# Performance work log

Hardware: AMD Instinct MI355X
Metric: run time of the kernel (lower is better)

## Reference

```python
import jax, jax.numpy as jnp
import numpy as np

TEMPERATURE = 8.0  # sqrt(d_head=64)


def setup_inputs() -> dict:
    key = jax.random.key(0)
    ks = jax.random.split(key, 6)
    shape = (4, 16, 2048, 64)  # [B, H, L, d_head]
    names = ["q_real", "q_imag", "k_real", "k_imag", "v_real", "v_imag"]
    return {n: jax.random.normal(k, shape, dtype=jnp.float32) for n, k in zip(names, ks)}


def reference(q_real, q_imag, k_real, k_imag, v_real, v_imag):
    # attn = | (q / T) @ conj(k)^H |
    # complex matmul with b = conj(k)^T: br = k_r^T, bi = -k_i^T
    qr = q_real / TEMPERATURE
    qi = q_imag / TEMPERATURE
    # [B,H,Lq,Lk]
    s_real = jnp.einsum("bhqd,bhkd->bhqk", qr, k_real) + jnp.einsum("bhqd,bhkd->bhqk", qi, k_imag)
    s_imag = jnp.einsum("bhqd,bhkd->bhqk", qi, k_real) - jnp.einsum("bhqd,bhkd->bhqk", qr, k_imag)
    attn = jax.nn.softmax(jnp.sqrt(s_real * s_real + s_imag * s_imag), axis=-1)
    # dropout p=0.0 (eval) -> identity
    out_real = jnp.einsum("bhqk,bhkd->bhqd", attn, v_real)
    out_imag = jnp.einsum("bhqk,bhkd->bhqd", attn, v_imag)
    # torch.view_as_complex(stack([real, imag], -1)) -> represent as stacked last dim
    output = jnp.stack([out_real, out_imag], axis=-1)  # [B,H,L,d,2]
    return output, attn
```

## Files before the change

### kernel.cpp

```cpp
#include <hip/hip_runtime.h>
#include <hip/hip_bf16.h>

constexpr int kL  = 2048;
constexpr int kD  = 64;
constexpr int kBH = 64;
constexpr size_t kAttnOff = (size_t)kBH * kL * kD * 2;

typedef __bf16 bf16x8 __attribute__((ext_vector_type(8)));
typedef __bf16 bf16x4 __attribute__((ext_vector_type(4)));
typedef float  f32x4  __attribute__((ext_vector_type(4)));
typedef unsigned int u32x4 __attribute__((ext_vector_type(4)));

static __device__ inline bf16x8 neg8(bf16x8 v) {
  u32x4 t = __builtin_bit_cast(u32x4, v);
  t ^= 0x80008000u;
  return __builtin_bit_cast(bf16x8, t);
}

static __device__ inline bf16x8 pack8(const float4& a, const float4& b) {
  bf16x8 p;
  p[0]=(__bf16)a.x; p[1]=(__bf16)a.y; p[2]=(__bf16)a.z; p[3]=(__bf16)a.w;
  p[4]=(__bf16)b.x; p[5]=(__bf16)b.y; p[6]=(__bf16)b.z; p[7]=(__bf16)b.w;
  return p;
}

__global__ __launch_bounds__(256) void transpose_v_kernel(
    const float* __restrict__ vr_g, const float* __restrict__ vi_g,
    __hip_bfloat16* __restrict__ vt_r, __hip_bfloat16* __restrict__ vt_i)
{
  __shared__ __align__(16) char lds_raw[2 * 8192];
  char* tr = lds_raw;
  char* ti = lds_raw + 8192;

  const int tid = threadIdx.x;
  const int bh  = blockIdx.x >> 5;
  const int kb  = blockIdx.x & 31;
  const int k0  = kb * 64;

  {
    const int krow = tid >> 2;
    const int d0   = (tid & 3) << 4;
    const size_t gb = ((size_t)bh * kL + k0 + krow) * kD + d0;
    const int base = krow * 128;
    const int swz  = (krow & 7) << 4;
    {
      float4 x0 = *(const float4*)(vr_g + gb);
      float4 x1 = *(const float4*)(vr_g + gb + 4);
      float4 x2 = *(const float4*)(vr_g + gb + 8);
      float4 x3 = *(const float4*)(vr_g + gb + 12);
      *(bf16x8*)(tr + base + ((d0 * 2) ^ swz))      = pack8(x0, x1);
      *(bf16x8*)(tr + base + ((d0 * 2 + 16) ^ swz)) = pack8(x2, x3);
    }
    {
      float4 y0 = *(const float4*)(vi_g + gb);
      float4 y1 = *(const float4*)(vi_g + gb + 4);
      float4 y2 = *(const float4*)(vi_g + gb + 8);
      float4 y3 = *(const float4*)(vi_g + gb + 12);
      *(bf16x8*)(ti + base + ((d0 * 2) ^ swz))      = pack8(y0, y1);
      *(bf16x8*)(ti + base + ((d0 * 2 + 16) ^ swz)) = pack8(y2, y3);
    }
  }
  __syncthreads();

  {
    const int d  = tid >> 2;
    const int kc = (tid & 3) << 4;
    const size_t tb = ((size_t)bh * 32 + kb) * 8192;
    char* outr = (char*)vt_r + tb + d * 128;
    char* outi = (char*)vt_i + tb + d * 128;
    const int oswz = (d & 7) << 4;
    bf16x8 pr0, pr1, pi0, pi1;
#pragma unroll
    for (int j = 0; j < 8; ++j) {
      const int k1 = kc + j;
      const int k2 = kc + 8 + j;
      const int b1 = k1 * 128 + ((d * 2) ^ ((k1 & 7) << 4));
      const int b2 = k2 * 128 + ((d * 2) ^ ((k2 & 7) << 4));
      pr0[j] = *(const __bf16*)(tr + b1);
      pr1[j] = *(const __bf16*)(tr + b2);
      pi0[j] = *(const __bf16*)(ti + b1);
      pi1[j] = *(const __bf16*)(ti + b2);
    }
    *(bf16x8*)(outr + ((kc * 2) ^ oswz))      = pr0;
    *(bf16x8*)(outr + ((kc * 2 + 16) ^ oswz)) = pr1;
    *(bf16x8*)(outi + ((kc * 2) ^ oswz))      = pi0;
    *(bf16x8*)(outi + ((kc * 2 + 16) ^ oswz)) = pi1;
  }
}

__global__ __launch_bounds__(256, 2) void fused_all(
    const float* __restrict__ qr_g, const float* __restrict__ qi_g,
    const float* __restrict__ kr_g, const float* __restrict__ ki_g,
    const __hip_bfloat16* __restrict__ vt_r, const __hip_bfloat16* __restrict__ vt_i,
    float* __restrict__ attn, float* __restrict__ out)
{
  __shared__ __align__(16) char lds_raw[49664];
  char*  e_l   = lds_raw + 32768 + (threadIdx.x >> 6) * 4096;
  float* inv_l = (float*)(lds_raw + 49152);

  const int tid  = threadIdx.x;
  const int wave = tid >> 6;
  const int lane = tid & 63;
  const int g    = lane >> 4;
  const int r    = lane & 15;

  const int bid = blockIdx.x;
  const int nid = (bid & 7) * 128 + (bid >> 3);
  const int bh  = nid >> 4;
  const int q0w = (nid & 15) * 128 + wave * 32;

  bf16x8 aqr[2][2], aqi[2][2];
#pragma unroll
  for (int qt = 0; qt < 2; ++qt) {
    const size_t qbase = ((size_t)bh * kL + q0w + qt * 16 + r) * kD + g * 8;
#pragma unroll
    for (int f = 0; f < 2; ++f) {
      float4 x0 = *(const float4*)(qr_g + qbase + f * 32);
      float4 x1 = *(const float4*)(qr_g + qbase + f * 32 + 4);
      float4 y0 = *(const float4*)(qi_g + qbase + f * 32);
      float4 y1 = *(const float4*)(qi_g + qbase + f * 32 + 4);
      float xr[8] = {x0.x, x0.y, x0.z, x0.w, x1.x, x1.y, x1.z, x1.w};
      float xi[8] = {y0.x, y0.y, y0.z, y0.w, y1.x, y1.y, y1.z, y1.w};
#pragma unroll
      for (int i = 0; i < 8; ++i) {
        aqr[qt][f][i] = (__bf16)(xr[i] * 0.125f);
        aqi[qt][f][i] = (__bf16)(xi[i] * 0.125f);
      }
    }
  }

  const int srow = tid >> 2;
  const int sd0  = (tid & 3) << 4;

  auto STAGE_K = [&](char* buf, int krow0) {
    const size_t gb = ((size_t)bh * kL + krow0 + srow) * kD + sd0;
    const int base = srow * 128;
    const int swz  = (srow & 7) << 4;
    float4 x0 = *(const float4*)(kr_g + gb);
    float4 x1 = *(const float4*)(kr_g + gb + 4);
    float4 x2 = *(const float4*)(kr_g + gb + 8);
    float4 x3 = *(const float4*)(kr_g + gb + 12);
    float4 y0 = *(const float4*)(ki_g + gb);
    float4 y1 = *(const float4*)(ki_g + gb + 4);
    float4 y2 = *(const float4*)(ki_g + gb + 8);
    float4 y3 = *(const float4*)(ki_g + gb + 12);
    *(bf16x8*)(buf + base + ((sd0 * 2) ^ swz))             = pack8(x0, x1);
    *(bf16x8*)(buf + base + ((sd0 * 2 + 16) ^ swz))        = pack8(x2, x3);
    *(bf16x8*)(buf + 8192 + base + ((sd0 * 2) ^ swz))      = pack8(y0, y1);
    *(bf16x8*)(buf + 8192 + base + ((sd0 * 2 + 16) ^ swz)) = pack8(y2, y3);
  };

  auto QK_E = [&](const char* kr_l, const char* ki_l, int s, int qt, float e[4]) {
    const int krow = s * 16 + r;
    const int swz  = (krow & 7) << 4;
    bf16x8 bkr[2], bki[2], bkin[2];
#pragma unroll
    for (int f = 0; f < 2; ++f) {
      const int byte = krow * 128 + (((f * 32 + g * 8) * 2) ^ swz);
      bkr[f]  = *(const bf16x8*)(kr_l + byte);
      bki[f]  = *(const bf16x8*)(ki_l + byte);
      bkin[f] = neg8(bki[f]);
    }
    f32x4 accr = {0.f, 0.f, 0.f, 0.f};
    f32x4 acci = {0.f, 0.f, 0.f, 0.f};
#pragma unroll
    for (int f = 0; f < 2; ++f) {
      accr = __builtin_amdgcn_mfma_f32_16x16x32_bf16(bkr[f],  aqr[qt][f], accr, 0, 0, 0);
      accr = __builtin_amdgcn_mfma_f32_16x16x32_bf16(bki[f],  aqi[qt][f], accr, 0, 0, 0);
      acci = __builtin_amdgcn_mfma_f32_16x16x32_bf16(bkr[f],  aqi[qt][f], acci, 0, 0, 0);
      acci = __builtin_amdgcn_mfma_f32_16x16x32_bf16(bkin[f], aqr[qt][f], acci, 0, 0, 0);
    }
#pragma unroll
    for (int i = 0; i < 4; ++i)
      e[i] = __expf(sqrtf(accr[i] * accr[i] + acci[i] * acci[i]));
  };

  float rs[2] = {0.f, 0.f};

#pragma unroll 1
  for (int t = 0; t < 16; ++t) {
    __syncthreads();
#pragma unroll
    for (int c = 0; c < 2; ++c) STAGE_K(lds_raw + c * 16384, t * 128 + c * 64);
    __syncthreads();
#pragma unroll
    for (int c = 0; c < 2; ++c) {
      const char* kr_l = lds_raw + c * 16384;
      const char* ki_l = kr_l + 8192;
#pragma unroll
      for (int s = 0; s < 4; ++s) {
#pragma unroll
        for (int qt = 0; qt < 2; ++qt) {
          float e[4];
          QK_E(kr_l, ki_l, s, qt, e);
          rs[qt] += (e[0] + e[1]) + (e[2] + e[3]);
        }
      }
    }
  }

#pragma unroll
  for (int qt = 0; qt < 2; ++qt) {
    rs[qt] += __shfl_xor(rs[qt], 16, 64);
    rs[qt] += __shfl_xor(rs[qt], 32, 64);
  }
  if (lane < 16) {
    inv_l[wave * 32 + lane]      = 1.0f / rs[0];
    inv_l[wave * 32 + 16 + lane] = 1.0f / rs[1];
  }

  f32x4 o_r[2][4], o_i[2][4];
#pragma unroll
  for (int qt = 0; qt < 2; ++qt)
#pragma unroll
    for (int dt = 0; dt < 4; ++dt) {
      o_r[qt][dt] = (f32x4){0.f, 0.f, 0.f, 0.f};
      o_i[qt][dt] = (f32x4){0.f, 0.f, 0.f, 0.f};
    }

#pragma unroll 1
  for (int t = 0; t < 32; ++t) {
    const int k0 = t * 64;
    __syncthreads();
    STAGE_K(lds_raw, k0);
    {
      const size_t tb = ((size_t)bh * 32 + t) * 8192;
      const int o1 = tid * 16;
      const int o2 = o1 + 4096;
      *(u32x4*)(lds_raw + 16384 + o1) = *(const u32x4*)((const char*)vt_r + tb + o1);
      *(u32x4*)(lds_raw + 16384 + o2) = *(const u32x4*)((const char*)vt_r + tb + o2);
      *(u32x4*)(lds_raw + 24576 + o1) = *(const u32x4*)((const char*)vt_i + tb + o1);
      *(u32x4*)(lds_raw + 24576 + o2) = *(const u32x4*)((const char*)vt_i + tb + o2);
    }
    __syncthreads();

#pragma unroll
    for (int s = 0; s < 4; ++s) {
#pragma unroll
      for (int qt = 0; qt < 2; ++qt) {
        float e[4];
        QK_E(lds_raw, lds_raw + 8192, s, qt, e);
        bf16x4 pe;
#pragma unroll
        for (int i = 0; i < 4; ++i) pe[i] = (__bf16)e[i];
        const int row = qt * 16 + r;
        *(bf16x4*)(e_l + row * 128 + (((s * 16 + g * 4) * 2) ^ ((row & 7) << 4))) = pe;
      }
    }

#pragma unroll
    for (int m = 0; m < 4; ++m) {
      const int row  = m * 8 + (lane >> 3);
      const int byte = row * 128 + (((lane & 7) * 16) ^ ((row & 7) << 4));
      bf16x8 v = *(const bf16x8*)(e_l + byte);
      const float inv = inv_l[wave * 32 + row];
      float4 w0, w1;
      w0.x = (float)v[0] * inv; w0.y = (float)v[1] * inv;
      w0.z = (float)v[2] * inv; w0.w = (float)v[3] * inv;
      w1.x = (float)v[4] * inv; w1.y = (float)v[5] * inv;
      w1.z = (float)v[6] * inv; w1.w = (float)v[7] * inv;
      const size_t base = ((size_t)bh * kL + q0w + row) * kL + k0 + (lane & 7) * 8;
      *(float4*)(attn + base)     = w0;
      *(float4*)(attn + base + 4) = w1;
    }

#pragma unroll
    for (int kh = 0; kh < 2; ++kh) {
      bf16x8 af[2];
#pragma unroll
      for (int qt = 0; qt < 2; ++qt) {
        const int row = qt * 16 + r;
        af[qt] = *(const bf16x8*)(e_l + row * 128 + (((kh * 32 + g * 8) * 2) ^ ((row & 7) << 4)));
      }
#pragma unroll
      for (int dt = 0; dt < 4; ++dt) {
        const int d = dt * 16 + r;
        const int byte = d * 128 + (((kh * 32 + g * 8) * 2) ^ ((d & 7) << 4));
        bf16x8 bvr = *(const bf16x8*)(lds_raw + 16384 + byte);
        bf16x8 bvi = *(const bf16x8*)(lds_raw + 24576 + byte);
#pragma unroll
        for (int qt = 0; qt < 2; ++qt) {
          o_r[qt][dt] = __builtin_amdgcn_mfma_f32_16x16x32_bf16(af[qt], bvr, o_r[qt][dt], 0, 0, 0);
          o_i[qt][dt] = __builtin_amdgcn_mfma_f32_16x16x32_bf16(af[qt], bvi, o_i[qt][dt], 0, 0, 0);
        }
      }
    }
  }

#pragma unroll
  for (int qt = 0; qt < 2; ++qt)
#pragma unroll
    for (int i = 0; i < 4; ++i) {
      const float sv = __shfl(rs[qt], g * 4 + i, 64);
      const float iv = 1.0f / sv;
      const size_t q = q0w + qt * 16 + g * 4 + i;
#pragma unroll
      for (int dt = 0; dt < 4; ++dt) {
        const int d = dt * 16 + r;
        float2 val;
        val.x = o_r[qt][dt][i] * iv;
        val.y = o_i[qt][dt][i] * iv;
        *(float2*)(out + (((size_t)bh * kL + q) * kD + d) * 2) = val;
      }
    }
}

__global__ __launch_bounds__(256) void qk_exp_legacy(
    const float* __restrict__ qr_g, const float* __restrict__ qi_g,
    const float* __restrict__ kr_g, const float* __restrict__ ki_g,
    float* __restrict__ attn, float* __restrict__ rowsum)
{
  __shared__ __align__(16) char lds_raw[16384 + 4 * 4096];
  char* kr_l = lds_raw;
  char* ki_l = lds_raw + 8192;
  char* e_l  = lds_raw + 16384 + (threadIdx.x >> 6) * 4096;

  const int tid  = threadIdx.x;
  const int wave = tid >> 6;
  const int lane = tid & 63;
  const int g    = lane >> 4;
  const int r    = lane & 15;

  const int bid = blockIdx.x;
  const int nid = (bid & 7) * 128 + (bid >> 3);
  const int bh  = nid >> 4;
  const int q0w = (nid & 15) * 128 + wave * 32;

  bf16x8 aqr[2][2], aqi[2][2];
#pragma unroll
  for (int qt = 0; qt < 2; ++qt) {
    const size_t qbase = ((size_t)bh * kL + q0w + qt * 16 + r) * kD + g * 8;
#pragma unroll
    for (int f = 0; f < 2; ++f) {
      float4 x0 = *(const float4*)(qr_g + qbase + f * 32);
      float4 x1 = *(const float4*)(qr_g + qbase + f * 32 + 4);
      float4 y0 = *(const float4*)(qi_g + qbase + f * 32);
      float4 y1 = *(const float4*)(qi_g + qbase + f * 32 + 4);
      float xr[8] = {x0.x, x0.y, x0.z, x0.w, x1.x, x1.y, x1.z, x1.w};
      float xi[8] = {y0.x, y0.y, y0.z, y0.w, y1.x, y1.y, y1.z, y1.w};
#pragma unroll
      for (int i = 0; i < 8; ++i) {
        aqr[qt][f][i] = (__bf16)(xr[i] * 0.125f);
        aqi[qt][f][i] = (__bf16)(xi[i] * 0.125f);
      }
    }
  }

  float rs[2] = {0.f, 0.f};

  for (int k0 = 0; k0 < kL; k0 += 64) {
    __syncthreads();
    {
      const int row = tid >> 2;
      const int d0  = (tid & 3) << 4;
      const size_t gb = ((size_t)bh * kL + k0 + row) * kD + d0;
      const int base = row * 128;
      const int swz  = (row & 7) << 4;
      {
        float4 x0 = *(const float4*)(kr_g + gb);
        float4 x1 = *(const float4*)(kr_g + gb + 4);
        float4 x2 = *(const float4*)(kr_g + gb + 8);
        float4 x3 = *(const float4*)(kr_g + gb + 12);
        *(bf16x8*)(kr_l + base + ((d0 * 2) ^ swz))      = pack8(x0, x1);
        *(bf16x8*)(kr_l + base + ((d0 * 2 + 16) ^ swz)) = pack8(x2, x3);
      }
      {
        float4 x0 = *(const float4*)(ki_g + gb);
        float4 x1 = *(const float4*)(ki_g + gb + 4);
        float4 x2 = *(const float4*)(ki_g + gb + 8);
        float4 x3 = *(const float4*)(ki_g + gb + 12);
        *(bf16x8*)(ki_l + base + ((d0 * 2) ^ swz))      = pack8(x0, x1);
        *(bf16x8*)(ki_l + base + ((d0 * 2 + 16) ^ swz)) = pack8(x2, x3);
      }
    }
    __syncthreads();

#pragma unroll
    for (int s = 0; s < 4; ++s) {
      const int krow = s * 16 + r;
      const int swz  = (krow & 7) << 4;
      bf16x8 bkr[2], bki[2], bkin[2];
#pragma unroll
      for (int f = 0; f < 2; ++f) {
        const int byte = krow * 128 + (((f * 32 + g * 8) * 2) ^ swz);
        bkr[f]  = *(const bf16x8*)(kr_l + byte);
        bki[f]  = *(const bf16x8*)(ki_l + byte);
        bkin[f] = neg8(bki[f]);
      }
#pragma unroll
      for (int qt = 0; qt < 2; ++qt) {
        f32x4 accr = {0.f, 0.f, 0.f, 0.f};
        f32x4 acci = {0.f, 0.f, 0.f, 0.f};
#pragma unroll
        for (int f = 0; f < 2; ++f) {
          accr = __builtin_amdgcn_mfma_f32_16x16x32_bf16(bkr[f],  aqr[qt][f], accr, 0, 0, 0);
          accr = __builtin_amdgcn_mfma_f32_16x16x32_bf16(bki[f],  aqi[qt][f], accr, 0, 0, 0);
          acci = __builtin_amdgcn_mfma_f32_16x16x32_bf16(bkr[f],  aqi[qt][f], acci, 0, 0, 0);
          acci = __builtin_amdgcn_mfma_f32_16x16x32_bf16(bkin[f], aqr[qt][f], acci, 0, 0, 0);
        }
        float e[4];
#pragma unroll
        for (int i = 0; i < 4; ++i)
          e[i] = __expf(sqrtf(accr[i] * accr[i] + acci[i] * acci[i]));
        rs[qt] += (e[0] + e[1]) + (e[2] + e[3]);
        bf16x4 pe;
#pragma unroll
        for (int i = 0; i < 4; ++i) pe[i] = (__bf16)e[i];
        const int row = qt * 16 + r;
        *(bf16x4*)(e_l + row * 128 + (((s * 16 + g * 4) * 2) ^ ((row & 7) << 4))) = pe;
      }
    }

#pragma unroll
    for (int m = 0; m < 4; ++m) {
      const int row  = m * 8 + (lane >> 3);
      const int byte = row * 128 + (((lane & 7) * 16) ^ ((row & 7) << 4));
      bf16x8 v = *(const bf16x8*)(e_l + byte);
      const size_t base = ((size_t)bh * kL + q0w + row) * kL + k0 + (lane & 7) * 8;
      float4 w0, w1;
      w0.x=(float)v[0]; w0.y=(float)v[1]; w0.z=(float)v[2]; w0.w=(float)v[3];
      w1.x=(float)v[4]; w1.y=(float)v[5]; w1.z=(float)v[6]; w1.w=(float)v[7];
      *(float4*)(attn + base)     = w0;
      *(float4*)(attn + base + 4) = w1;
    }
  }

#pragma unroll
  for (int qt = 0; qt < 2; ++qt) {
    rs[qt] += __shfl_xor(rs[qt], 16, 64);
    rs[qt] += __shfl_xor(rs[qt], 32, 64);
  }
  if (lane < 16) {
#pragma unroll
    for (int qt = 0; qt < 2; ++qt)
      rowsum[(size_t)bh * kL + q0w + qt * 16 + lane] = rs[qt];
  }
}

__global__ __launch_bounds__(256) void pv_legacy(
    const float* __restrict__ vr_g, const float* __restrict__ vi_g,
    float* __restrict__ attn, const float* __restrict__ rowsum,
    float* __restrict__ out)
{
  __shared__ __align__(16) char lds_raw[2 * 8192];
  char* vr_l = lds_raw;
  char* vi_l = lds_raw + 8192;

  const int tid  = threadIdx.x;
  const int wave = tid >> 6;
  const int lane = tid & 63;
  const int g    = lane >> 4;
  const int r    = lane & 15;

  const int bid = blockIdx.x;
  const int nid = (bid & 7) * 128 + (bid >> 3);
  const int bh  = nid >> 4;
  const int q0w = (nid & 15) * 128 + wave * 32;

  float invA[2];
#pragma unroll
  for (int qt = 0; qt < 2; ++qt)
    invA[qt] = 1.0f / rowsum[(size_t)bh * kL + q0w + qt * 16 + r];

  f32x4 o_r[2][4], o_i[2][4];
#pragma unroll
  for (int qt = 0; qt < 2; ++qt)
#pragma unroll
    for (int dt = 0; dt < 4; ++dt) {
      o_r[qt][dt] = (f32x4){0.f, 0.f, 0.f, 0.f};
      o_i[qt][dt] = (f32x4){0.f, 0.f, 0.f, 0.f};
    }

  for (int k0 = 0; k0 < kL; k0 += 64) {
    __syncthreads();
    {
      const int p  = tid >> 3;
      const int d0 = (tid & 7) << 3;
      const size_t gb0 = ((size_t)bh * kL + k0 + 2 * p) * kD + d0;
      const size_t gb1 = gb0 + kD;
      float4 a0 = *(const float4*)(vr_g + gb0);
      float4 a1 = *(const float4*)(vr_g + gb0 + 4);
      float4 a2 = *(const float4*)(vr_g + gb1);
      float4 a3 = *(const float4*)(vr_g + gb1 + 4);
      float4 b0 = *(const float4*)(vi_g + gb0);
      float4 b1 = *(const float4*)(vi_g + gb0 + 4);
      float4 b2 = *(const float4*)(vi_g + gb1);
      float4 b3 = *(const float4*)(vi_g + gb1 + 4);
      float vr0[8] = {a0.x, a0.y, a0.z, a0.w, a1.x, a1.y, a1.z, a1.w};
      float vr1[8] = {a2.x, a2.y, a2.z, a2.w, a3.x, a3.y, a3.z, a3.w};
      float vi0[8] = {b0.x, b0.y, b0.z, b0.w, b1.x, b1.y, b1.z, b1.w};
      float vi1[8] = {b2.x, b2.y, b2.z, b2.w, b3.x, b3.y, b3.z, b3.w};
#pragma unroll
      for (int j = 0; j < 8; ++j) {
        const int d = d0 + j;
        const int byte = d * 128 + ((p * 4) ^ ((d & 7) << 4));
        __bf16 pa[2] = {(__bf16)vr0[j], (__bf16)vr1[j]};
        __bf16 pb[2] = {(__bf16)vi0[j], (__bf16)vi1[j]};
        *(unsigned int*)(vr_l + byte) = *(unsigned int*)pa;
        *(unsigned int*)(vi_l + byte) = *(unsigned int*)pb;
      }
    }
    __syncthreads();

#pragma unroll
    for (int kh = 0; kh < 2; ++kh) {
      bf16x8 af[2];
#pragma unroll
      for (int qt = 0; qt < 2; ++qt) {
        const size_t q = q0w + qt * 16 + r;
        const size_t eb = ((size_t)bh * kL + q) * kL + k0 + kh * 32 + g * 8;
        float4 e0 = *(const float4*)(attn + eb);
        float4 e1 = *(const float4*)(attn + eb + 4);
        af[qt][0]=(__bf16)e0.x; af[qt][1]=(__bf16)e0.y; af[qt][2]=(__bf16)e0.z; af[qt][3]=(__bf16)e0.w;
        af[qt][4]=(__bf16)e1.x; af[qt][5]=(__bf16)e1.y; af[qt][6]=(__bf16)e1.z; af[qt][7]=(__bf16)e1.w;
        float4 w0 = {e0.x * invA[qt], e0.y * invA[qt], e0.z * invA[qt], e0.w * invA[qt]};
        float4 w1 = {e1.x * invA[qt], e1.y * invA[qt], e1.z * invA[qt], e1.w * invA[qt]};
        *(float4*)(attn + eb)     = w0;
        *(float4*)(attn + eb + 4) = w1;
      }
#pragma unroll
      for (int dt = 0; dt < 4; ++dt) {
        const int d = dt * 16 + r;
        const int byte = d * 128 + (((kh * 32 + g * 8) * 2) ^ ((d & 7) << 4));
        bf16x8 bvr = *(const bf16x8*)(vr_l + byte);
        bf16x8 bvi = *(const bf16x8*)(vi_l + byte);
#pragma unroll
        for (int qt = 0; qt < 2; ++qt) {
          o_r[qt][dt] = __builtin_amdgcn_mfma_f32_16x16x32_bf16(af[qt], bvr, o_r[qt][dt], 0, 0, 0);
          o_i[qt][dt] = __builtin_amdgcn_mfma_f32_16x16x32_bf16(af[qt], bvi, o_i[qt][dt], 0, 0, 0);
        }
      }
    }
  }

#pragma unroll
  for (int qt = 0; qt < 2; ++qt)
#pragma unroll
    for (int i = 0; i < 4; ++i) {
      const size_t q = q0w + qt * 16 + g * 4 + i;
      const float iv = 1.0f / rowsum[(size_t)bh * kL + q];
#pragma unroll
      for (int dt = 0; dt < 4; ++dt) {
        const int d = dt * 16 + r;
        float2 val;
        val.x = o_r[qt][dt][i] * iv;
        val.y = o_i[qt][dt][i] * iv;
        *(float2*)(out + (((size_t)bh * kL + q) * kD + d) * 2) = val;
      }
    }
}

extern "C" void kernel_launch(void* const* d_in, const int* in_sizes, int n_in,
                              void* d_out, int out_size, void* d_ws, size_t ws_size,
                              hipStream_t stream) {
  const float* qr = (const float*)d_in[0];
  const float* qi = (const float*)d_in[1];
  const float* kr = (const float*)d_in[2];
  const float* ki = (const float*)d_in[3];
  const float* vr = (const float*)d_in[4];
  const float* vi = (const float*)d_in[5];
  float* out  = (float*)d_out;
  float* attn = out + kAttnOff;

  const size_t vt_bytes = (size_t)kBH * kD * kL * 2;
  __hip_bfloat16* vt_r = (__hip_bfloat16*)d_ws;
  __hip_bfloat16* vt_i = vt_r + (size_t)kBH * kD * kL;

  dim3 gridT(kBH * (kL / 64));
  dim3 gridM(kBH * (kL / 128));

  if (ws_size >= 2 * vt_bytes) {
    transpose_v_kernel<<<gridT, 256, 0, stream>>>(vr, vi, vt_r, vt_i);
    fused_all<<<gridM, 256, 0, stream>>>(qr, qi, kr, ki, vt_r, vt_i, attn, out);
  } else {
    float* rowsum = (float*)d_ws;
    qk_exp_legacy<<<gridM, 256, 0, stream>>>(qr, qi, kr, ki, attn, rowsum);
    pv_legacy<<<gridM, 256, 0, stream>>>(vr, vi, attn, rowsum, out);
  }
}
```

Measured before the change: 840.1 us.

## Drop rowsum pre-pass; write unnormalized bf16 exp and normalize in separate kernel

Removes the first QK pass that only computed softmax row sums, so QK and exp run once per tile. Unnormalized exp values go to a bf16 workspace, and a new kernel scales them by the row sums and writes the fp32 attention matrix. K is pre-converted to swizzled bf16 tiles in the prep kernel, and the fused kernel issues its tile loads before the barrier and raises occupancy to 3 blocks per CU. The cost is an extra bf16 round trip of the full attention matrix (512 MB write plus read) and a workspace that must hold it; if the workspace is too small, the legacy path runs instead.

```diff
diff --git a/kernel.cpp b/kernel.cpp
--- a/kernel.cpp
+++ b/kernel.cpp
@@ -24,8 +24,10 @@
   return p;
 }
 
-__global__ __launch_bounds__(256) void transpose_v_kernel(
+__global__ __launch_bounds__(256) void prep_kernel(
+    const float* __restrict__ kr_g, const float* __restrict__ ki_g,
     const float* __restrict__ vr_g, const float* __restrict__ vi_g,
+    __hip_bfloat16* __restrict__ kb_r, __hip_bfloat16* __restrict__ kb_i,
     __hip_bfloat16* __restrict__ vt_r, __hip_bfloat16* __restrict__ vt_i)
 {
   __shared__ __align__(16) char lds_raw[2 * 8192];
@@ -36,36 +38,46 @@
   const int bh  = blockIdx.x >> 5;
   const int kb  = blockIdx.x & 31;
   const int k0  = kb * 64;
+  const size_t tb = ((size_t)bh * 32 + kb) * 8192;
+
+  const int row = tid >> 2;
+  const int d0  = (tid & 3) << 4;
+  const size_t gb = ((size_t)bh * kL + k0 + row) * kD + d0;
+  const int swz = (row & 7) << 4;
 
   {
-    const int krow = tid >> 2;
-    const int d0   = (tid & 3) << 4;
-    const size_t gb = ((size_t)bh * kL + k0 + krow) * kD + d0;
-    const int base = krow * 128;
-    const int swz  = (krow & 7) << 4;
-    {
-      float4 x0 = *(const float4*)(vr_g + gb);
-      float4 x1 = *(const float4*)(vr_g + gb + 4);
-      float4 x2 = *(const float4*)(vr_g + gb + 8);
-      float4 x3 = *(const float4*)(vr_g + gb + 12);
-      *(bf16x8*)(tr + base + ((d0 * 2) ^ swz))      = pack8(x0, x1);
-      *(bf16x8*)(tr + base + ((d0 * 2 + 16) ^ swz)) = pack8(x2, x3);
-    }
-    {
-      float4 y0 = *(const float4*)(vi_g + gb);
-      float4 y1 = *(const float4*)(vi_g + gb + 4);
-      float4 y2 = *(const float4*)(vi_g + gb + 8);
-      float4 y3 = *(const float4*)(vi_g + gb + 12);
-      *(bf16x8*)(ti + base + ((d0 * 2) ^ swz))      = pack8(y0, y1);
-      *(bf16x8*)(ti + base + ((d0 * 2 + 16) ^ swz)) = pack8(y2, y3);
-    }
+    float4 x0 = *(const float4*)(kr_g + gb);
+    float4 x1 = *(const float4*)(kr_g + gb + 4);
+    float4 x2 = *(const float4*)(kr_g + gb + 8);
+    float4 x3 = *(const float4*)(kr_g + gb + 12);
+    *(bf16x8*)((char*)kb_r + tb + row * 128 + ((d0 * 2) ^ swz))      = pack8(x0, x1);
+    *(bf16x8*)((char*)kb_r + tb + row * 128 + ((d0 * 2 + 16) ^ swz)) = pack8(x2, x3);
+    float4 y0 = *(const float4*)(ki_g + gb);
+    float4 y1 = *(const float4*)(ki_g + gb + 4);
+    float4 y2 = *(const float4*)(ki_g + gb + 8);
+    float4 y3 = *(const float4*)(ki_g + gb + 12);
+    *(bf16x8*)((char*)kb_i + tb + row * 128 + ((d0 * 2) ^ swz))      = pack8(y0, y1);
+    *(bf16x8*)((char*)kb_i + tb + row * 128 + ((d0 * 2 + 16) ^ swz)) = pack8(y2, y3);
+  }
+
+  {
+    float4 x0 = *(const float4*)(vr_g + gb);
+    float4 x1 = *(const float4*)(vr_g + gb + 4);
+    float4 x2 = *(const float4*)(vr_g + gb + 8);
+    float4 x3 = *(const float4*)(vr_g + gb + 12);
+    *(bf16x8*)(tr + row * 128 + ((d0 * 2) ^ swz))      = pack8(x0, x1);
+    *(bf16x8*)(tr + row * 128 + ((d0 * 2 + 16) ^ swz)) = pack8(x2, x3);
+    float4 y0 = *(const float4*)(vi_g + gb);
+    float4 y1 = *(const float4*)(vi_g + gb + 4);
+    float4 y2 = *(const float4*)(vi_g + gb + 8);
+    float4 y3 = *(const float4*)(vi_g + gb + 12);
+    *(bf16x8*)(ti + row * 128 + ((d0 * 2) ^ swz))      = pack8(y0, y1);
+    *(bf16x8*)(ti + row * 128 + ((d0 * 2 + 16) ^ swz)) = pack8(y2, y3);
   }
   __syncthreads();
-
   {
     const int d  = tid >> 2;
     const int kc = (tid & 3) << 4;
-    const size_t tb = ((size_t)bh * 32 + kb) * 8192;
     char* outr = (char*)vt_r + tb + d * 128;
     char* outi = (char*)vt_i + tb + d * 128;
     const int oswz = (d & 7) << 4;
@@ -88,15 +100,15 @@
   }
 }
 
-__global__ __launch_bounds__(256, 2) void fused_all(
+__global__ __launch_bounds__(256, 3) void fused_qkpv(
     const float* __restrict__ qr_g, const float* __restrict__ qi_g,
-    const float* __restrict__ kr_g, const float* __restrict__ ki_g,
+    const __hip_bfloat16* __restrict__ kb_r, const __hip_bfloat16* __restrict__ kb_i,
     const __hip_bfloat16* __restrict__ vt_r, const __hip_bfloat16* __restrict__ vt_i,
-    float* __restrict__ attn, float* __restrict__ out)
+    __hip_bfloat16* __restrict__ ews, float* __restrict__ rowsum,
+    float* __restrict__ out)
 {
-  __shared__ __align__(16) char lds_raw[49664];
-  char*  e_l   = lds_raw + 32768 + (threadIdx.x >> 6) * 4096;
-  float* inv_l = (float*)(lds_raw + 49152);
+  __shared__ __align__(16) char lds_raw[49152];
+  char* e_l = lds_raw + 32768 + (threadIdx.x >> 6) * 4096;
 
   const int tid  = threadIdx.x;
   const int wave = tid >> 6;
@@ -109,7 +121,7 @@
   const int bh  = nid >> 4;
   const int q0w = (nid & 15) * 128 + wave * 32;
 
-  bf16x8 aqr[2][2], aqi[2][2];
+  bf16x8 aqr[2][2], aqi[2][2], aqrn[2][2];
 #pragma unroll
   for (int qt = 0; qt < 2; ++qt) {
     const size_t qbase = ((size_t)bh * kL + q0w + qt * 16 + r) * kD + g * 8;
@@ -126,89 +138,11 @@
         aqr[qt][f][i] = (__bf16)(xr[i] * 0.125f);
         aqi[qt][f][i] = (__bf16)(xi[i] * 0.125f);
       }
-    }
-  }
-
-  const int srow = tid >> 2;
-  const int sd0  = (tid & 3) << 4;
-
-  auto STAGE_K = [&](char* buf, int krow0) {
-    const size_t gb = ((size_t)bh * kL + krow0 + srow) * kD + sd0;
-    const int base = srow * 128;
-    const int swz  = (srow & 7) << 4;
-    float4 x0 = *(const float4*)(kr_g + gb);
-    float4 x1 = *(const float4*)(kr_g + gb + 4);
-    float4 x2 = *(const float4*)(kr_g + gb + 8);
-    float4 x3 = *(const float4*)(kr_g + gb + 12);
-    float4 y0 = *(const float4*)(ki_g + gb);
-    float4 y1 = *(const float4*)(ki_g + gb + 4);
-    float4 y2 = *(const float4*)(ki_g + gb + 8);
-    float4 y3 = *(const float4*)(ki_g + gb + 12);
-    *(bf16x8*)(buf + base + ((sd0 * 2) ^ swz))             = pack8(x0, x1);
-    *(bf16x8*)(buf + base + ((sd0 * 2 + 16) ^ swz))        = pack8(x2, x3);
-    *(bf16x8*)(buf + 8192 + base + ((sd0 * 2) ^ swz))      = pack8(y0, y1);
-    *(bf16x8*)(buf + 8192 + base + ((sd0 * 2 + 16) ^ swz)) = pack8(y2, y3);
-  };
-
-  auto QK_E = [&](const char* kr_l, const char* ki_l, int s, int qt, float e[4]) {
-    const int krow = s * 16 + r;
-    const int swz  = (krow & 7) << 4;
-    bf16x8 bkr[2], bki[2], bkin[2];
-#pragma unroll
-    for (int f = 0; f < 2; ++f) {
-      const int byte = krow * 128 + (((f * 32 + g * 8) * 2) ^ swz);
-      bkr[f]  = *(const bf16x8*)(kr_l + byte);
-      bki[f]  = *(const bf16x8*)(ki_l + byte);
-      bkin[f] = neg8(bki[f]);
-    }
-    f32x4 accr = {0.f, 0.f, 0.f, 0.f};
-    f32x4 acci = {0.f, 0.f, 0.f, 0.f};
-#pragma unroll
-    for (int f = 0; f < 2; ++f) {
-      accr = __builtin_amdgcn_mfma_f32_16x16x32_bf16(bkr[f],  aqr[qt][f], accr, 0, 0, 0);
-      accr = __builtin_amdgcn_mfma_f32_16x16x32_bf16(bki[f],  aqi[qt][f], accr, 0, 0, 0);
-      acci = __builtin_amdgcn_mfma_f32_16x16x32_bf16(bkr[f],  aqi[qt][f], acci, 0, 0, 0);
-      acci = __builtin_amdgcn_mfma_f32_16x16x32_bf16(bkin[f], aqr[qt][f], acci, 0, 0, 0);
-    }
-#pragma unroll
-    for (int i = 0; i < 4; ++i)
-      e[i] = __expf(sqrtf(accr[i] * accr[i] + acci[i] * acci[i]));
-  };
+      aqrn[qt][f] = neg8(aqr[qt][f]);
+    }
+  }
 
   float rs[2] = {0.f, 0.f};
-
-#pragma unroll 1
-  for (int t = 0; t < 16; ++t) {
-    __syncthreads();
-#pragma unroll
-    for (int c = 0; c < 2; ++c) STAGE_K(lds_raw + c * 16384, t * 128 + c * 64);
-    __syncthreads();
-#pragma unroll
-    for (int c = 0; c < 2; ++c) {
-      const char* kr_l = lds_raw + c * 16384;
-      const char* ki_l = kr_l + 8192;
-#pragma unroll
-      for (int s = 0; s < 4; ++s) {
-#pragma unroll
-        for (int qt = 0; qt < 2; ++qt) {
-          float e[4];
-          QK_E(kr_l, ki_l, s, qt, e);
-          rs[qt] += (e[0] + e[1]) + (e[2] + e[3]);
-        }
-      }
-    }
-  }
-
-#pragma unroll
-  for (int qt = 0; qt < 2; ++qt) {
-    rs[qt] += __shfl_xor(rs[qt], 16, 64);
-    rs[qt] += __shfl_xor(rs[qt], 32, 64);
-  }
-  if (lane < 16) {
-    inv_l[wave * 32 + lane]      = 1.0f / rs[0];
-    inv_l[wave * 32 + 16 + lane] = 1.0f / rs[1];
-  }
-
   f32x4 o_r[2][4], o_i[2][4];
 #pragma unroll
   for (int qt = 0; qt < 2; ++qt)
@@ -218,28 +152,60 @@
       o_i[qt][dt] = (f32x4){0.f, 0.f, 0.f, 0.f};
     }
 
+  const int off1 = tid * 16;
+  const int off2 = off1 + 4096;
+
 #pragma unroll 1
   for (int t = 0; t < 32; ++t) {
     const int k0 = t * 64;
+    const size_t tb = ((size_t)bh * 32 + t) * 8192;
+
+    u32x4 a0 = *(const u32x4*)((const char*)kb_r + tb + off1);
+    u32x4 a1 = *(const u32x4*)((const char*)kb_r + tb + off2);
+    u32x4 b0 = *(const u32x4*)((const char*)kb_i + tb + off1);
+    u32x4 b1 = *(const u32x4*)((const char*)kb_i + tb + off2);
+    u32x4 c0 = *(const u32x4*)((const char*)vt_r + tb + off1);
+    u32x4 c1 = *(const u32x4*)((const char*)vt_r + tb + off2);
+    u32x4 d0 = *(const u32x4*)((const char*)vt_i + tb + off1);
+    u32x4 d1 = *(const u32x4*)((const char*)vt_i + tb + off2);
     __syncthreads();
-    STAGE_K(lds_raw, k0);
-    {
-      const size_t tb = ((size_t)bh * 32 + t) * 8192;
-      const int o1 = tid * 16;
-      const int o2 = o1 + 4096;
-      *(u32x4*)(lds_raw + 16384 + o1) = *(const u32x4*)((const char*)vt_r + tb + o1);
-      *(u32x4*)(lds_raw + 16384 + o2) = *(const u32x4*)((const char*)vt_r + tb + o2);
-      *(u32x4*)(lds_raw + 24576 + o1) = *(const u32x4*)((const char*)vt_i + tb + o1);
-      *(u32x4*)(lds_raw + 24576 + o2) = *(const u32x4*)((const char*)vt_i + tb + o2);
-    }
+    *(u32x4*)(lds_raw + off1)         = a0;
+    *(u32x4*)(lds_raw + off2)         = a1;
+    *(u32x4*)(lds_raw + 8192 + off1)  = b0;
+    *(u32x4*)(lds_raw + 8192 + off2)  = b1;
+    *(u32x4*)(lds_raw + 16384 + off1) = c0;
+    *(u32x4*)(lds_raw + 16384 + off2) = c1;
+    *(u32x4*)(lds_raw + 24576 + off1) = d0;
+    *(u32x4*)(lds_raw + 24576 + off2) = d1;
     __syncthreads();
 
 #pragma unroll
     for (int s = 0; s < 4; ++s) {
+      const int krow = s * 16 + r;
+      const int swz  = (krow & 7) << 4;
+      bf16x8 bkr[2], bki[2];
+#pragma unroll
+      for (int f = 0; f < 2; ++f) {
+        const int byte = krow * 128 + (((f * 32 + g * 8) * 2) ^ swz);
+        bkr[f] = *(const bf16x8*)(lds_raw + byte);
+        bki[f] = *(const bf16x8*)(lds_raw + 8192 + byte);
+      }
 #pragma unroll
       for (int qt = 0; qt < 2; ++qt) {
+        f32x4 accr = {0.f, 0.f, 0.f, 0.f};
+        f32x4 acci = {0.f, 0.f, 0.f, 0.f};
+#pragma unroll
+        for (int f = 0; f < 2; ++f) {
+          accr = __builtin_amdgcn_mfma_f32_16x16x32_bf16(bkr[f], aqr[qt][f],  accr, 0, 0, 0);
+          accr = __builtin_amdgcn_mfma_f32_16x16x32_bf16(bki[f], aqi[qt][f],  accr, 0, 0, 0);
+          acci = __builtin_amdgcn_mfma_f32_16x16x32_bf16(bkr[f], aqi[qt][f],  acci, 0, 0, 0);
+          acci = __builtin_amdgcn_mfma_f32_16x16x32_bf16(bki[f], aqrn[qt][f], acci, 0, 0, 0);
+        }
         float e[4];
-        QK_E(lds_raw, lds_raw + 8192, s, qt, e);
+#pragma unroll
+        for (int i = 0; i < 4; ++i)
+          e[i] = __expf(sqrtf(accr[i] * accr[i] + acci[i] * acci[i]));
+        rs[qt] += (e[0] + e[1]) + (e[2] + e[3]);
         bf16x4 pe;
 #pragma unroll
         for (int i = 0; i < 4; ++i) pe[i] = (__bf16)e[i];
@@ -253,15 +219,8 @@
       const int row  = m * 8 + (lane >> 3);
       const int byte = row * 128 + (((lane & 7) * 16) ^ ((row & 7) << 4));
       bf16x8 v = *(const bf16x8*)(e_l + byte);
-      const float inv = inv_l[wave * 32 + row];
-      float4 w0, w1;
-      w0.x = (float)v[0] * inv; w0.y = (float)v[1] * inv;
-      w0.z = (float)v[2] * inv; w0.w = (float)v[3] * inv;
-      w1.x = (float)v[4] * inv; w1.y = (float)v[5] * inv;
-      w1.z = (float)v[6] * inv; w1.w = (float)v[7] * inv;
       const size_t base = ((size_t)bh * kL + q0w + row) * kL + k0 + (lane & 7) * 8;
-      *(float4*)(attn + base)     = w0;
-      *(float4*)(attn + base + 4) = w1;
+      *(bf16x8*)((__bf16*)ews + base) = v;
     }
 
 #pragma unroll
@@ -285,6 +244,17 @@
         }
       }
     }
+  }
+
+#pragma unroll
+  for (int qt = 0; qt < 2; ++qt) {
+    rs[qt] += __shfl_xor(rs[qt], 16, 64);
+    rs[qt] += __shfl_xor(rs[qt], 32, 64);
+  }
+  if (lane < 16) {
+#pragma unroll
+    for (int qt = 0; qt < 2; ++qt)
+      rowsum[(size_t)bh * kL + q0w + qt * 16 + lane] = rs[qt];
   }
 
 #pragma unroll
@@ -303,6 +273,30 @@
         *(float2*)(out + (((size_t)bh * kL + q) * kD + d) * 2) = val;
       }
     }
+}
+
+__global__ __launch_bounds__(256) void norm_kernel(
+    const __hip_bfloat16* __restrict__ ews, float* __restrict__ attn,
+    const float* __restrict__ rowsum)
+{
+  const int wave = threadIdx.x >> 6;
+  const int lane = threadIdx.x & 63;
+  const int row  = blockIdx.x * 4 + wave;
+  const float inv = 1.0f / rowsum[row];
+  const size_t base = (size_t)row * kL;
+
+#pragma unroll
+  for (int j = 0; j < 4; ++j) {
+    const size_t off = base + j * 512 + lane * 8;
+    bf16x8 v = *(const bf16x8*)((const __bf16*)ews + off);
+    float4 w0, w1;
+    w0.x = (float)v[0] * inv; w0.y = (float)v[1] * inv;
+    w0.z = (float)v[2] * inv; w0.w = (float)v[3] * inv;
+    w1.x = (float)v[4] * inv; w1.y = (float)v[5] * inv;
+    w1.z = (float)v[6] * inv; w1.w = (float)v[7] * inv;
+    *(float4*)(attn + off)     = w0;
+    *(float4*)(attn + off + 4) = w1;
+  }
 }
 
 __global__ __launch_bounds__(256) void qk_exp_legacy(
@@ -562,19 +556,27 @@
   float* out  = (float*)d_out;
   float* attn = out + kAttnOff;
 
-  const size_t vt_bytes = (size_t)kBH * kD * kL * 2;
-  __hip_bfloat16* vt_r = (__hip_bfloat16*)d_ws;
-  __hip_bfloat16* vt_i = vt_r + (size_t)kBH * kD * kL;
-
-  dim3 gridT(kBH * (kL / 64));
-  dim3 gridM(kBH * (kL / 128));
-
-  if (ws_size >= 2 * vt_bytes) {
-    transpose_v_kernel<<<gridT, 256, 0, stream>>>(vr, vi, vt_r, vt_i);
-    fused_all<<<gridM, 256, 0, stream>>>(qr, qi, kr, ki, vt_r, vt_i, attn, out);
+  const size_t rowsum_bytes = (size_t)kBH * kL * 4;
+  const size_t e_bytes      = (size_t)kBH * kL * kL * 2;
+  const size_t tile_bytes   = (size_t)kBH * kL * kD * 2;
+  float* rowsum = (float*)d_ws;
+  __hip_bfloat16* ews  = (__hip_bfloat16*)((char*)d_ws + rowsum_bytes);
+  char* tiles = (char*)d_ws + rowsum_bytes + e_bytes;
+  __hip_bfloat16* kb_r = (__hip_bfloat16*)(tiles);
+  __hip_bfloat16* kb_i = (__hip_bfloat16*)(tiles + tile_bytes);
+  __hip_bfloat16* vt_r = (__hip_bfloat16*)(tiles + 2 * tile_bytes);
+  __hip_bfloat16* vt_i = (__hip_bfloat16*)(tiles + 3 * tile_bytes);
+
+  dim3 gridP(kBH * (kL / 64));
+  dim3 gridF(kBH * (kL / 128));
+  dim3 gridN(kBH * kL / 4);
+
+  if (ws_size >= rowsum_bytes + e_bytes + 4 * tile_bytes) {
+    prep_kernel<<<gridP, 256, 0, stream>>>(kr, ki, vr, vi, kb_r, kb_i, vt_r, vt_i);
+    fused_qkpv<<<gridF, 256, 0, stream>>>(qr, qi, kb_r, kb_i, vt_r, vt_i, ews, rowsum, out);
+    norm_kernel<<<gridN, 256, 0, stream>>>(ews, attn, rowsum);
   } else {
-    float* rowsum = (float*)d_ws;
-    qk_exp_legacy<<<gridM, 256, 0, stream>>>(qr, qi, kr, ki, attn, rowsum);
-    pv_legacy<<<gridM, 256, 0, stream>>>(vr, vi, attn, rowsum, out);
-  }
-}
+    qk_exp_legacy<<<gridF, 256, 0, stream>>>(qr, qi, kr, ki, attn, rowsum);
+    pv_legacy<<<gridF, 256, 0, stream>>>(vr, vi, attn, rowsum, out);
+  }
+}
```

Result: slower. 867.9 us (+3.3%).
